# Performance work log

Measured on AMD Instinct MI355X. Metric: run time of the kernel, lower is better.

## Reference

```python
import jax, jax.numpy as jnp
import numpy as np

ND, NM = 20000, 80000
N = ND + NM
IN_D = 256
IN_M = 256
HID = 128
OUT2 = 128  # out_channels * 2
E = 1_600_000
E_TEST = 1_000_000


def setup_inputs() -> dict:
    key = jax.random.key(0)
    ks = jax.random.split(key, 12)
    xd = jax.random.normal(ks[0], (ND, IN_D), jnp.float32)
    xm = jax.random.normal(ks[1], (NM, IN_M), jnp.float32)
    # mlp1: Linear(IN_D, HID); mlp2: Linear(IN_M, HID); gcn: GCNConv(HID, OUT2)
    W1 = jax.random.normal(ks[2], (IN_D, HID), jnp.float32) / np.sqrt(IN_D)
    b1 = jnp.zeros((HID,), jnp.float32)
    W2 = jax.random.normal(ks[3], (IN_M, HID), jnp.float32) / np.sqrt(IN_M)
    b2 = jnp.zeros((HID,), jnp.float32)
    Wg = jax.random.normal(ks[4], (HID, OUT2), jnp.float32) / np.sqrt(HID)
    bg = jnp.zeros((OUT2,), jnp.float32)
    edge_index = jax.random.randint(ks[5], (2, E), 0, N, dtype=jnp.int64)
    edge_index_test = jax.random.randint(ks[6], (2, E_TEST), 0, N, dtype=jnp.int64)
    return dict(xd=xd, xm=xm, edge_index=edge_index, edge_index_test=edge_index_test,
                W1=W1, b1=b1, W2=W2, b2=b2, Wg=Wg, bg=bg)


def gcn_conv(x, edge_index, W, b, num_nodes):
    """PyG GCNConv: x' = D^{-1/2}(A+I)D^{-1/2} x W + b, self-loops added."""
    src, dst = edge_index[0], edge_index[1]
    h = x @ W  # [N, out]
    # degree of A + I (edge weight 1), counted at destination
    deg = jnp.ones((num_nodes,), x.dtype).at[dst].add(1.0)
    norm = jax.lax.rsqrt(deg)
    coef = (norm[src] * norm[dst])[:, None]           # [E,1]
    agg = jax.ops.segment_sum(h[src] * coef, dst, num_segments=num_nodes)
    agg = agg + h * (norm * norm)[:, None]            # self-loop term
    return agg + b


def reference(xd, xm, edge_index, edge_index_test, W1, b1, W2, b2, Wg, bg):
    hd = jax.nn.relu(xd @ W1 + b1)                    # [ND, HID]
    hm = jax.nn.relu(xm @ W2 + b2)                    # [NM, HID]
    x = jnp.concatenate([hd, hm], axis=0)             # [N, HID]
    x = jax.nn.relu(gcn_conv(x, edge_index, Wg, bg, N))  # [N, OUT2]
    # edge dot-product scoring
    scores = jnp.sum(x[edge_index_test[0]] * x[edge_index_test[1]], axis=-1)
    return scores
```

## Files before the change

kernel.cpp:

```cpp
#include <hip/hip_runtime.h>
#include <cstddef>


typedef __attribute__((ext_vector_type(8))) short short8;
typedef __attribute__((ext_vector_type(4))) float f32x4;

#define NBUCK_MAX 2048

__device__ __forceinline__ unsigned short f2bf(float f) {
  union { float f; unsigned u; } v;
  v.f = f;
  unsigned r = v.u + 0x7fffu + ((v.u >> 16) & 1u);
  return (unsigned short)(r >> 16);
}
__device__ __forceinline__ float bf2f(short s) {
  union { unsigned u; float f; } v;
  v.u = ((unsigned)(unsigned short)s) << 16;
  return v.f;
}

__device__ __forceinline__ int eidx(const void* p, int f64, long long i) {
  if (f64) return (int)((const long long*)p)[i];
  return ((const int*)p)[i];
}

__global__ void detect_kernel(const void* __restrict__ ei,
                              const void* __restrict__ eit,
                              int* __restrict__ flags) {
  const unsigned* a = (const unsigned*)ei;
  const unsigned* b = (const unsigned*)eit;
  int f1 = 1, f2 = 1;
  for (int i = 0; i < 64; ++i) {
    if (a[2 * i + 1] != 0u) f1 = 0;
    if (b[2 * i + 1] != 0u) f2 = 0;
  }
  flags[0] = f1;
  flags[1] = f2;
}

__global__ __launch_bounds__(256) void bucket_hist_kernel(
    const void* __restrict__ ei, const int* __restrict__ flags,
    int* __restrict__ bcnt, int E, int nbuck) {
  __shared__ int h[NBUCK_MAX];
  for (int i = threadIdx.x; i < nbuck; i += 256) h[i] = 0;
  __syncthreads();
  int f = flags[0];
  int stride = gridDim.x * 256;
  for (long long e = blockIdx.x * 256 + threadIdx.x; e < E; e += stride) {
    int d = eidx(ei, f, (long long)E + e);
    atomicAdd(&h[d >> 8], 1);
  }
  __syncthreads();
  for (int i = threadIdx.x; i < nbuck; i += 256) {
    int c = h[i];
    if (c) atomicAdd(&bcnt[i], c);
  }
}

__global__ __launch_bounds__(1024) void bucket_scan_kernel(
    const int* __restrict__ bcnt, int* __restrict__ bbase,
    int* __restrict__ bcursor, int nbuck) {
  __shared__ int s[1024];
  int t = threadIdx.x;
  int v = (t < nbuck) ? bcnt[t] : 0;
  s[t] = v;
  __syncthreads();
#pragma unroll
  for (int off = 1; off < 1024; off <<= 1) {
    int x = (t >= off) ? s[t - off] : 0;
    __syncthreads();
    s[t] += x;
    __syncthreads();
  }
  if (t < nbuck) {
    int e = s[t] - v;
    bbase[t] = e;
    bcursor[t] = e;
  }
}

template <int C>
__global__ __launch_bounds__(256) void bin_kernel(
    const void* __restrict__ ei, const int* __restrict__ flags,
    int* __restrict__ bcursor, int* __restrict__ stg, int E, int nbuck) {
  __shared__ int hcnt[NBUCK_MAX];
  __shared__ int hbase[NBUCK_MAX];
  for (int i = threadIdx.x; i < nbuck; i += 256) hcnt[i] = 0;
  __syncthreads();
  int f = flags[0];
  int pk[C], bk[C];
  long long base = (long long)blockIdx.x * 256 * C;
#pragma unroll
  for (int j = 0; j < C; ++j) {
    long long e = base + j * 256 + threadIdx.x;
    if (e < E) {
      int s = eidx(ei, f, e);
      int d = eidx(ei, f, (long long)E + e);
      bk[j] = d >> 8;
      pk[j] = s | ((d & 255) << 20);
      atomicAdd(&hcnt[bk[j]], 1);
    } else {
      bk[j] = -1;
    }
  }
  __syncthreads();
  for (int i = threadIdx.x; i < nbuck; i += 256) {
    int c = hcnt[i];
    hbase[i] = c ? atomicAdd(&bcursor[i], c) : 0;
    hcnt[i] = 0;
  }
  __syncthreads();
#pragma unroll
  for (int j = 0; j < C; ++j) {
    if (bk[j] >= 0) {
      int r = atomicAdd(&hcnt[bk[j]], 1);
      stg[hbase[bk[j]] + r] = pk[j];
    }
  }
}

__global__ __launch_bounds__(256) void sortfin_kernel(
    const int* __restrict__ stg, const int* __restrict__ bbase,
    const int* __restrict__ bcnt, int* __restrict__ sorted_src,
    int* __restrict__ offsets, int* __restrict__ count,
    float* __restrict__ norm, int N) {
  int b = blockIdx.x;
  int start = bbase[b];
  int len = bcnt[b];
  __shared__ int ncnt[256];
  __shared__ int ncur[256];
  __shared__ int stmp[256];
  int t = threadIdx.x;
  ncnt[t] = 0;
  __syncthreads();
  for (int i = t; i < len; i += 256) {
    int p = stg[start + i];
    atomicAdd(&ncnt[p >> 20], 1);
  }
  __syncthreads();
  int c = ncnt[t];
  stmp[t] = c;
  __syncthreads();
#pragma unroll
  for (int off = 1; off < 256; off <<= 1) {
    int x = (t >= off) ? stmp[t - off] : 0;
    __syncthreads();
    stmp[t] += x;
    __syncthreads();
  }
  int aoff = start + stmp[t] - c;
  ncur[t] = aoff;
  int node = (b << 8) + t;
  if (node < N) {
    offsets[node] = aoff;
    count[node] = c;
    norm[node] = rsqrtf((float)c + 1.0f);
  }
  __syncthreads();
  for (int i = t; i < len; i += 256) {
    int p = stg[start + i];
    int pos = atomicAdd(&ncur[p >> 20], 1);
    sorted_src[pos] = p & 0xFFFFF;
  }
}

__global__ void wtrans_all_kernel(const float* __restrict__ W1,
                                  const float* __restrict__ W2,
                                  const float* __restrict__ Wg,
                                  unsigned short* __restrict__ WT1,
                                  unsigned short* __restrict__ WT2,
                                  unsigned short* __restrict__ WTg) {
  int b = blockIdx.x;
  const float* W;
  unsigned short* WT;
  int K, n;
  if (b < 128) {
    W = W1; WT = WT1; K = 256; n = b;
  } else if (b < 256) {
    W = W2; WT = WT2; K = 256; n = b - 128;
  } else {
    W = Wg; WT = WTg; K = 128; n = b - 256;
  }
  for (int k = threadIdx.x; k < K; k += blockDim.x)
    WT[(size_t)n * K + k] = f2bf(W[(size_t)k * 128 + n]);
}

template <int K, bool BF16IN, bool RELU>
__device__ __forceinline__ void gemm_body(const void* __restrict__ Xv,
                                          const unsigned short* __restrict__ WT,
                                          const float* __restrict__ bias,
                                          unsigned short* __restrict__ Yb,
                                          int M, int m0) {
  __shared__ short As[128][40];
  __shared__ short Bs[128][40];

  const int tid = threadIdx.x;
  const int lane = tid & 63;
  const int wave = tid >> 6;
  const int wr = wave >> 1, wc = wave & 1;
  const int lrow = lane & 15;
  const int lk = (lane >> 4) * 8;

  f32x4 acc[4][4];
#pragma unroll
  for (int i = 0; i < 4; ++i)
#pragma unroll
    for (int j = 0; j < 4; ++j) acc[i][j] = (f32x4)(0.0f);

  const int srow = tid >> 1;
  const int skh = (tid & 1) * 16;

  for (int k0 = 0; k0 < K; k0 += 32) {
    {
      int grow = m0 + srow;
      short8 p0 = (short8)(0), p1 = (short8)(0);
      if (grow < M) {
        if (BF16IN) {
          const short* Xb = (const short*)Xv;
          p0 = *(const short8*)&Xb[(size_t)grow * K + k0 + skh];
          p1 = *(const short8*)&Xb[(size_t)grow * K + k0 + skh + 8];
        } else {
          const float* Xf = (const float*)Xv;
          const float4* xp = (const float4*)&Xf[(size_t)grow * K + k0 + skh];
          float4 v0 = xp[0], v1 = xp[1], v2 = xp[2], v3 = xp[3];
          p0[0] = (short)f2bf(v0.x); p0[1] = (short)f2bf(v0.y);
          p0[2] = (short)f2bf(v0.z); p0[3] = (short)f2bf(v0.w);
          p0[4] = (short)f2bf(v1.x); p0[5] = (short)f2bf(v1.y);
          p0[6] = (short)f2bf(v1.z); p0[7] = (short)f2bf(v1.w);
          p1[0] = (short)f2bf(v2.x); p1[1] = (short)f2bf(v2.y);
          p1[2] = (short)f2bf(v2.z); p1[3] = (short)f2bf(v2.w);
          p1[4] = (short)f2bf(v3.x); p1[5] = (short)f2bf(v3.y);
          p1[6] = (short)f2bf(v3.z); p1[7] = (short)f2bf(v3.w);
        }
      }
      *(short8*)&As[srow][skh] = p0;
      *(short8*)&As[srow][skh + 8] = p1;
    }
    {
      const short* wt = (const short*)WT;
      short8 q0 = *(const short8*)&wt[(size_t)srow * K + k0 + skh];
      short8 q1 = *(const short8*)&wt[(size_t)srow * K + k0 + skh + 8];
      *(short8*)&Bs[srow][skh] = q0;
      *(short8*)&Bs[srow][skh + 8] = q1;
    }
    __syncthreads();

    short8 a[4], b[4];
#pragma unroll
    for (int f = 0; f < 4; ++f) {
      a[f] = *(const short8*)&As[wr * 64 + f * 16 + lrow][lk];
      b[f] = *(const short8*)&Bs[wc * 64 + f * 16 + lrow][lk];
    }
#pragma unroll
    for (int fm = 0; fm < 4; ++fm)
#pragma unroll
      for (int fn = 0; fn < 4; ++fn)
        acc[fm][fn] = __builtin_amdgcn_mfma_f32_16x16x32_bf16(
            a[fm], b[fn], acc[fm][fn], 0, 0, 0);
    __syncthreads();
  }

#pragma unroll
  for (int fm = 0; fm < 4; ++fm) {
    int rbase = m0 + wr * 64 + fm * 16 + (lane >> 4) * 4;
#pragma unroll
    for (int fn = 0; fn < 4; ++fn) {
      int col = wc * 64 + fn * 16 + lrow;
      float bv = RELU ? bias[col] : 0.0f;
      f32x4 v = acc[fm][fn];
#pragma unroll
      for (int r = 0; r < 4; ++r) {
        int grow = rbase + r;
        if (grow < M) {
          float x = v[r];
          if (RELU) x = fmaxf(x + bv, 0.0f);
          Yb[(size_t)grow * 128 + col] = f2bf(x);
        }
      }
    }
  }
}

__global__ __launch_bounds__(256) void mlp_gemm_kernel(
    const float* __restrict__ xd, const float* __restrict__ xm,
    const unsigned short* __restrict__ WT1,
    const unsigned short* __restrict__ WT2, const float* __restrict__ b1,
    const float* __restrict__ b2, unsigned short* __restrict__ h, int ND,
    int NM, int nbd) {
  if ((int)blockIdx.x < nbd) {
    gemm_body<256, false, true>(xd, WT1, b1, h, ND, blockIdx.x * 128);
  } else {
    gemm_body<256, false, true>(xm, WT2, b2, h + (size_t)ND * 128, NM,
                                (blockIdx.x - nbd) * 128);
  }
}

__global__ __launch_bounds__(256) void gcn_gemm_kernel(
    const short* __restrict__ h, const unsigned short* __restrict__ WTg,
    unsigned short* __restrict__ h2, int N) {
  gemm_body<128, true, false>(h, WTg, nullptr, h2, N, blockIdx.x * 128);
}

__global__ __launch_bounds__(256) void gather_agg_kernel(
    const short* __restrict__ h2, const float* __restrict__ norm,
    const int* __restrict__ offsets, const int* __restrict__ count,
    const int* __restrict__ sorted_src, const float* __restrict__ bg,
    short* __restrict__ x2, int N) {
  int t = blockIdx.x * blockDim.x + threadIdx.x;
  int node = t >> 3;
  if (node >= N) return;
  int l = t & 7;

  float nd = norm[node];
  int start = offsets[node];
  int len = count[node];

  float a[16];
  {
    short8 s0 = *(const short8*)&h2[(size_t)node * 128 + l * 16];
    short8 s1 = *(const short8*)&h2[(size_t)node * 128 + l * 16 + 8];
    float nw = nd * nd;
#pragma unroll
    for (int i = 0; i < 8; ++i) {
      a[i] = bf2f(s0[i]) * nw;
      a[8 + i] = bf2f(s1[i]) * nw;
    }
  }

  int j = 0;
  for (; j + 2 <= len; j += 2) {
    int sA = sorted_src[start + j];
    int sB = sorted_src[start + j + 1];
    float cA = norm[sA] * nd;
    float cB = norm[sB] * nd;
    const short* pA = &h2[(size_t)sA * 128 + l * 16];
    const short* pB = &h2[(size_t)sB * 128 + l * 16];
    short8 vA0 = *(const short8*)pA;
    short8 vA1 = *(const short8*)(pA + 8);
    short8 vB0 = *(const short8*)pB;
    short8 vB1 = *(const short8*)(pB + 8);
#pragma unroll
    for (int i = 0; i < 8; ++i) {
      a[i] += cA * bf2f(vA0[i]) + cB * bf2f(vB0[i]);
      a[8 + i] += cA * bf2f(vA1[i]) + cB * bf2f(vB1[i]);
    }
  }
  if (j < len) {
    int sA = sorted_src[start + j];
    float cA = norm[sA] * nd;
    const short* pA = &h2[(size_t)sA * 128 + l * 16];
    short8 vA0 = *(const short8*)pA;
    short8 vA1 = *(const short8*)(pA + 8);
#pragma unroll
    for (int i = 0; i < 8; ++i) {
      a[i] += cA * bf2f(vA0[i]);
      a[8 + i] += cA * bf2f(vA1[i]);
    }
  }

  short8 o0, o1;
#pragma unroll
  for (int i = 0; i < 8; ++i) {
    o0[i] = (short)f2bf(fmaxf(a[i] + bg[l * 16 + i], 0.0f));
    o1[i] = (short)f2bf(fmaxf(a[8 + i] + bg[l * 16 + 8 + i], 0.0f));
  }
  *(short8*)&x2[(size_t)node * 128 + l * 16] = o0;
  *(short8*)&x2[(size_t)node * 128 + l * 16 + 8] = o1;
}

__global__ __launch_bounds__(256) void score_kernel(
    const short* __restrict__ x2, const void* __restrict__ eit,
    const int* __restrict__ flags, float* __restrict__ out, int ET) {
  int t = blockIdx.x * blockDim.x + threadIdx.x;
  int e = t >> 3;
  if (e >= ET) return;
  int l = t & 7;
  int f = flags[1];
  int s = eidx(eit, f, e);
  int d = eidx(eit, f, (long long)ET + e);
  const short* pa = &x2[(size_t)s * 128 + l * 16];
  const short* pb = &x2[(size_t)d * 128 + l * 16];
  short8 a0 = *(const short8*)pa;
  short8 a1 = *(const short8*)(pa + 8);
  short8 b0 = *(const short8*)pb;
  short8 b1 = *(const short8*)(pb + 8);
  float p = 0.0f;
#pragma unroll
  for (int i = 0; i < 8; ++i)
    p += bf2f(a0[i]) * bf2f(b0[i]) + bf2f(a1[i]) * bf2f(b1[i]);
  p += __shfl_xor(p, 4);
  p += __shfl_xor(p, 2);
  p += __shfl_xor(p, 1);
  if (l == 0) out[e] = p;
}

extern "C" void kernel_launch(void* const* d_in, const int* in_sizes, int n_in,
                              void* d_out, int out_size, void* d_ws,
                              size_t ws_size, hipStream_t stream) {
  const float* xd = (const float*)d_in[0];
  const float* xm = (const float*)d_in[1];
  const void* ei = d_in[2];
  const void* eit = d_in[3];
  const float* W1 = (const float*)d_in[4];
  const float* b1 = (const float*)d_in[5];
  const float* W2 = (const float*)d_in[6];
  const float* b2 = (const float*)d_in[7];
  const float* Wg = (const float*)d_in[8];
  const float* bg = (const float*)d_in[9];

  const int ND = in_sizes[0] / 256;
  const int NM = in_sizes[1] / 256;
  const int N = ND + NM;
  const int E = in_sizes[2] / 2;
  const int ET = in_sizes[3] / 2;
  const int nbuck = (N + 255) >> 8;

  float* out = (float*)d_out;

  char* p = (char*)d_ws;
  float* norm = (float*)p;        p += (size_t)N * 4;
  int* count = (int*)p;           p += (size_t)N * 4;
  int* offsets = (int*)p;         p += (size_t)N * 4;
  int* bcnt = (int*)p;            p += NBUCK_MAX * 4;
  int* bbase = (int*)p;           p += NBUCK_MAX * 4;
  int* bcursor = (int*)p;         p += NBUCK_MAX * 4;
  int* flags = (int*)p;           p += 16 * 4;
  int* stg = (int*)p;             p += (size_t)E * 4;
  int* sorted_src = (int*)p;      p += (size_t)E * 4;
  p = (char*)(((uintptr_t)p + 15) & ~(uintptr_t)15);
  short* h = (short*)p;           p += (size_t)N * 128 * 2;
  short* h2 = (short*)p;          p += (size_t)N * 128 * 2;
  unsigned short* WT1 = (unsigned short*)p; p += 128 * 256 * 2;
  unsigned short* WT2 = (unsigned short*)p; p += 128 * 256 * 2;
  unsigned short* WTg = (unsigned short*)p; p += 128 * 128 * 2;

  detect_kernel<<<1, 1, 0, stream>>>(ei, eit, flags);
  hipMemsetAsync(bcnt, 0, (size_t)nbuck * 4, stream);

  bucket_hist_kernel<<<256, 256, 0, stream>>>(ei, flags, bcnt, E, nbuck);
  bucket_scan_kernel<<<1, 1024, 0, stream>>>(bcnt, bbase, bcursor, nbuck);
  {
    constexpr int C = 16;
    int nblk = (int)(((long long)E + 256 * C - 1) / (256 * C));
    bin_kernel<C><<<nblk, 256, 0, stream>>>(ei, flags, bcursor, stg, E, nbuck);
  }
  sortfin_kernel<<<nbuck, 256, 0, stream>>>(stg, bbase, bcnt, sorted_src,
                                            offsets, count, norm, N);

  wtrans_all_kernel<<<384, 256, 0, stream>>>(W1, W2, Wg, WT1, WT2, WTg);

  {
    int nbd = (ND + 127) / 128;
    int nbm = (NM + 127) / 128;
    mlp_gemm_kernel<<<nbd + nbm, 256, 0, stream>>>(
        xd, xm, WT1, WT2, b1, b2, (unsigned short*)h, ND, NM, nbd);
  }
  gcn_gemm_kernel<<<(N + 127) / 128, 256, 0, stream>>>(
      h, WTg, (unsigned short*)h2, N);

  {
    long long tt = (long long)N * 8;
    gather_agg_kernel<<<(unsigned)((tt + 255) / 256), 256, 0, stream>>>(
        h2, norm, offsets, count, sorted_src, bg, h, N);
  }

  {
    long long tt = (long long)ET * 8;
    score_kernel<<<(unsigned)((tt + 255) / 256), 256, 0, stream>>>(h, eit, flags,
                                                                   out, ET);
  }
}
```

Before: 298.9 us.

## Co-schedule CSR sort stages with GEMMs via block-range fused kernels

Independent graph-preprocessing stages are merged into the GEMM launches using block-index ranges. Weight transpose and flag detection go in one kernel that also zeroes the bucket counts, replacing the memset. The destination histogram runs alongside the MLP GEMM, and edge binning runs alongside the GCN GEMM. The aggregation loop is also unrolled to four neighbours for more memory parallelism. This cuts launch count and lets memory-bound sorting overlap compute-bound GEMMs, at the cost of larger shared-memory footprints per fused kernel, which may lower occupancy.

```diff
diff --git a/kernel.cpp b/kernel.cpp
--- a/kernel.cpp
+++ b/kernel.cpp
@@ -24,165 +24,40 @@
   return ((const int*)p)[i];
 }
 
-__global__ void detect_kernel(const void* __restrict__ ei,
-                              const void* __restrict__ eit,
-                              int* __restrict__ flags) {
-  const unsigned* a = (const unsigned*)ei;
-  const unsigned* b = (const unsigned*)eit;
-  int f1 = 1, f2 = 1;
-  for (int i = 0; i < 64; ++i) {
-    if (a[2 * i + 1] != 0u) f1 = 0;
-    if (b[2 * i + 1] != 0u) f2 = 0;
-  }
-  flags[0] = f1;
-  flags[1] = f2;
-}
-
-__global__ __launch_bounds__(256) void bucket_hist_kernel(
-    const void* __restrict__ ei, const int* __restrict__ flags,
-    int* __restrict__ bcnt, int E, int nbuck) {
-  __shared__ int h[NBUCK_MAX];
-  for (int i = threadIdx.x; i < nbuck; i += 256) h[i] = 0;
-  __syncthreads();
-  int f = flags[0];
-  int stride = gridDim.x * 256;
-  for (long long e = blockIdx.x * 256 + threadIdx.x; e < E; e += stride) {
-    int d = eidx(ei, f, (long long)E + e);
-    atomicAdd(&h[d >> 8], 1);
-  }
-  __syncthreads();
-  for (int i = threadIdx.x; i < nbuck; i += 256) {
-    int c = h[i];
-    if (c) atomicAdd(&bcnt[i], c);
-  }
-}
-
-__global__ __launch_bounds__(1024) void bucket_scan_kernel(
-    const int* __restrict__ bcnt, int* __restrict__ bbase,
-    int* __restrict__ bcursor, int nbuck) {
-  __shared__ int s[1024];
+__global__ __launch_bounds__(256) void k0_kernel(
+    const float* __restrict__ W1, const float* __restrict__ W2,
+    const float* __restrict__ Wg, unsigned short* __restrict__ WT1,
+    unsigned short* __restrict__ WT2, unsigned short* __restrict__ WTg,
+    const void* __restrict__ ei, const void* __restrict__ eit,
+    int* __restrict__ flags, int* __restrict__ bcnt, int nbuck) {
+  int b = blockIdx.x;
   int t = threadIdx.x;
-  int v = (t < nbuck) ? bcnt[t] : 0;
-  s[t] = v;
-  __syncthreads();
-#pragma unroll
-  for (int off = 1; off < 1024; off <<= 1) {
-    int x = (t >= off) ? s[t - off] : 0;
-    __syncthreads();
-    s[t] += x;
-    __syncthreads();
-  }
-  if (t < nbuck) {
-    int e = s[t] - v;
-    bbase[t] = e;
-    bcursor[t] = e;
-  }
-}
-
-template <int C>
-__global__ __launch_bounds__(256) void bin_kernel(
-    const void* __restrict__ ei, const int* __restrict__ flags,
-    int* __restrict__ bcursor, int* __restrict__ stg, int E, int nbuck) {
-  __shared__ int hcnt[NBUCK_MAX];
-  __shared__ int hbase[NBUCK_MAX];
-  for (int i = threadIdx.x; i < nbuck; i += 256) hcnt[i] = 0;
-  __syncthreads();
-  int f = flags[0];
-  int pk[C], bk[C];
-  long long base = (long long)blockIdx.x * 256 * C;
-#pragma unroll
-  for (int j = 0; j < C; ++j) {
-    long long e = base + j * 256 + threadIdx.x;
-    if (e < E) {
-      int s = eidx(ei, f, e);
-      int d = eidx(ei, f, (long long)E + e);
-      bk[j] = d >> 8;
-      pk[j] = s | ((d & 255) << 20);
-      atomicAdd(&hcnt[bk[j]], 1);
+  if (b < 384) {
+    const float* W;
+    unsigned short* WT;
+    int K, n;
+    if (b < 128) {
+      W = W1; WT = WT1; K = 256; n = b;
+    } else if (b < 256) {
+      W = W2; WT = WT2; K = 256; n = b - 128;
     } else {
-      bk[j] = -1;
-    }
-  }
-  __syncthreads();
-  for (int i = threadIdx.x; i < nbuck; i += 256) {
-    int c = hcnt[i];
-    hbase[i] = c ? atomicAdd(&bcursor[i], c) : 0;
-    hcnt[i] = 0;
-  }
-  __syncthreads();
-#pragma unroll
-  for (int j = 0; j < C; ++j) {
-    if (bk[j] >= 0) {
-      int r = atomicAdd(&hcnt[bk[j]], 1);
-      stg[hbase[bk[j]] + r] = pk[j];
-    }
-  }
-}
-
-__global__ __launch_bounds__(256) void sortfin_kernel(
-    const int* __restrict__ stg, const int* __restrict__ bbase,
-    const int* __restrict__ bcnt, int* __restrict__ sorted_src,
-    int* __restrict__ offsets, int* __restrict__ count,
-    float* __restrict__ norm, int N) {
-  int b = blockIdx.x;
-  int start = bbase[b];
-  int len = bcnt[b];
-  __shared__ int ncnt[256];
-  __shared__ int ncur[256];
-  __shared__ int stmp[256];
-  int t = threadIdx.x;
-  ncnt[t] = 0;
-  __syncthreads();
-  for (int i = t; i < len; i += 256) {
-    int p = stg[start + i];
-    atomicAdd(&ncnt[p >> 20], 1);
-  }
-  __syncthreads();
-  int c = ncnt[t];
-  stmp[t] = c;
-  __syncthreads();
-#pragma unroll
-  for (int off = 1; off < 256; off <<= 1) {
-    int x = (t >= off) ? stmp[t - off] : 0;
-    __syncthreads();
-    stmp[t] += x;
-    __syncthreads();
-  }
-  int aoff = start + stmp[t] - c;
-  ncur[t] = aoff;
-  int node = (b << 8) + t;
-  if (node < N) {
-    offsets[node] = aoff;
-    count[node] = c;
-    norm[node] = rsqrtf((float)c + 1.0f);
-  }
-  __syncthreads();
-  for (int i = t; i < len; i += 256) {
-    int p = stg[start + i];
-    int pos = atomicAdd(&ncur[p >> 20], 1);
-    sorted_src[pos] = p & 0xFFFFF;
-  }
-}
-
-__global__ void wtrans_all_kernel(const float* __restrict__ W1,
-                                  const float* __restrict__ W2,
-                                  const float* __restrict__ Wg,
-                                  unsigned short* __restrict__ WT1,
-                                  unsigned short* __restrict__ WT2,
-                                  unsigned short* __restrict__ WTg) {
-  int b = blockIdx.x;
-  const float* W;
-  unsigned short* WT;
-  int K, n;
-  if (b < 128) {
-    W = W1; WT = WT1; K = 256; n = b;
-  } else if (b < 256) {
-    W = W2; WT = WT2; K = 256; n = b - 128;
+      W = Wg; WT = WTg; K = 128; n = b - 256;
+    }
+    for (int k = t; k < K; k += 256)
+      WT[(size_t)n * K + k] = f2bf(W[(size_t)k * 128 + n]);
   } else {
-    W = Wg; WT = WTg; K = 128; n = b - 256;
-  }
-  for (int k = threadIdx.x; k < K; k += blockDim.x)
-    WT[(size_t)n * K + k] = f2bf(W[(size_t)k * 128 + n]);
+    __shared__ int s1, s2;
+    if (t == 0) { s1 = 1; s2 = 1; }
+    __syncthreads();
+    if (t < 64) {
+      if (((const unsigned*)ei)[2 * t + 1] != 0u) s1 = 0;
+    } else if (t < 128) {
+      if (((const unsigned*)eit)[2 * (t - 64) + 1] != 0u) s2 = 0;
+    }
+    __syncthreads();
+    if (t == 0) { flags[0] = s1; flags[1] = s2; }
+    for (int i = t; i < nbuck; i += 256) bcnt[i] = 0;
+  }
 }
 
 template <int K, bool BF16IN, bool RELU>
@@ -281,24 +156,159 @@
   }
 }
 
-__global__ __launch_bounds__(256) void mlp_gemm_kernel(
+__global__ __launch_bounds__(256) void k1_kernel(
     const float* __restrict__ xd, const float* __restrict__ xm,
     const unsigned short* __restrict__ WT1,
     const unsigned short* __restrict__ WT2, const float* __restrict__ b1,
     const float* __restrict__ b2, unsigned short* __restrict__ h, int ND,
-    int NM, int nbd) {
-  if ((int)blockIdx.x < nbd) {
-    gemm_body<256, false, true>(xd, WT1, b1, h, ND, blockIdx.x * 128);
+    int NM, int nbd, int nbm, const void* __restrict__ ei,
+    const int* __restrict__ flags, int* __restrict__ bcnt, int E, int nbuck) {
+  int b = blockIdx.x;
+  int nmlp = nbd + nbm;
+  if (b < nbd) {
+    gemm_body<256, false, true>(xd, WT1, b1, h, ND, b * 128);
+  } else if (b < nmlp) {
+    gemm_body<256, false, true>(xm, WT2, b2, h + (size_t)ND * 128, NM,
+                                (b - nbd) * 128);
   } else {
-    gemm_body<256, false, true>(xm, WT2, b2, h + (size_t)ND * 128, NM,
-                                (blockIdx.x - nbd) * 128);
-  }
-}
-
-__global__ __launch_bounds__(256) void gcn_gemm_kernel(
+    int rb = b - nmlp;
+    __shared__ int hsh[NBUCK_MAX];
+    for (int i = threadIdx.x; i < nbuck; i += 256) hsh[i] = 0;
+    __syncthreads();
+    int f = flags[0];
+    long long stride = 256LL * 256;
+    for (long long e = (long long)rb * 256 + threadIdx.x; e < E; e += stride) {
+      int d = eidx(ei, f, (long long)E + e);
+      atomicAdd(&hsh[d >> 8], 1);
+    }
+    __syncthreads();
+    for (int i = threadIdx.x; i < nbuck; i += 256) {
+      int c = hsh[i];
+      if (c) atomicAdd(&bcnt[i], c);
+    }
+  }
+}
+
+__global__ __launch_bounds__(1024) void bucket_scan_kernel(
+    const int* __restrict__ bcnt, int* __restrict__ bbase,
+    int* __restrict__ bcursor, int nbuck) {
+  __shared__ int s[1024];
+  int t = threadIdx.x;
+  int v = (t < nbuck) ? bcnt[t] : 0;
+  s[t] = v;
+  __syncthreads();
+#pragma unroll
+  for (int off = 1; off < 1024; off <<= 1) {
+    int x = (t >= off) ? s[t - off] : 0;
+    __syncthreads();
+    s[t] += x;
+    __syncthreads();
+  }
+  if (t < nbuck) {
+    int e = s[t] - v;
+    bbase[t] = e;
+    bcursor[t] = e;
+  }
+}
+
+template <int C>
+__device__ __forceinline__ void bin_body(const void* __restrict__ ei,
+                                         const int* __restrict__ flags,
+                                         int* __restrict__ bcursor,
+                                         int* __restrict__ stg, int E,
+                                         int nbuck, int rb) {
+  __shared__ int hcnt[NBUCK_MAX];
+  __shared__ int hbase[NBUCK_MAX];
+  for (int i = threadIdx.x; i < nbuck; i += 256) hcnt[i] = 0;
+  __syncthreads();
+  int f = flags[0];
+  int pk[C], bk[C];
+  long long base = (long long)rb * 256 * C;
+#pragma unroll
+  for (int j = 0; j < C; ++j) {
+    long long e = base + j * 256 + threadIdx.x;
+    if (e < E) {
+      int s = eidx(ei, f, e);
+      int d = eidx(ei, f, (long long)E + e);
+      bk[j] = d >> 8;
+      pk[j] = s | ((d & 255) << 20);
+      atomicAdd(&hcnt[bk[j]], 1);
+    } else {
+      bk[j] = -1;
+    }
+  }
+  __syncthreads();
+  for (int i = threadIdx.x; i < nbuck; i += 256) {
+    int c = hcnt[i];
+    hbase[i] = c ? atomicAdd(&bcursor[i], c) : 0;
+    hcnt[i] = 0;
+  }
+  __syncthreads();
+#pragma unroll
+  for (int j = 0; j < C; ++j) {
+    if (bk[j] >= 0) {
+      int r = atomicAdd(&hcnt[bk[j]], 1);
+      stg[hbase[bk[j]] + r] = pk[j];
+    }
+  }
+}
+
+__global__ __launch_bounds__(256) void k3_kernel(
     const short* __restrict__ h, const unsigned short* __restrict__ WTg,
-    unsigned short* __restrict__ h2, int N) {
-  gemm_body<128, true, false>(h, WTg, nullptr, h2, N, blockIdx.x * 128);
+    unsigned short* __restrict__ h2, int N, int ngcn,
+    const void* __restrict__ ei, const int* __restrict__ flags,
+    int* __restrict__ bcursor, int* __restrict__ stg, int E, int nbuck) {
+  int b = blockIdx.x;
+  if (b < ngcn) {
+    gemm_body<128, true, false>((const void*)h, WTg, nullptr, h2, N, b * 128);
+  } else {
+    bin_body<16>(ei, flags, bcursor, stg, E, nbuck, b - ngcn);
+  }
+}
+
+__global__ __launch_bounds__(256) void sortfin_kernel(
+    const int* __restrict__ stg, const int* __restrict__ bbase,
+    const int* __restrict__ bcnt, int* __restrict__ sorted_src,
+    int* __restrict__ offsets, int* __restrict__ count,
+    float* __restrict__ norm, int N) {
+  int b = blockIdx.x;
+  int start = bbase[b];
+  int len = bcnt[b];
+  __shared__ int ncnt[256];
+  __shared__ int ncur[256];
+  __shared__ int stmp[256];
+  int t = threadIdx.x;
+  ncnt[t] = 0;
+  __syncthreads();
+  for (int i = t; i < len; i += 256) {
+    int p = stg[start + i];
+    atomicAdd(&ncnt[p >> 20], 1);
+  }
+  __syncthreads();
+  int c = ncnt[t];
+  stmp[t] = c;
+  __syncthreads();
+#pragma unroll
+  for (int off = 1; off < 256; off <<= 1) {
+    int x = (t >= off) ? stmp[t - off] : 0;
+    __syncthreads();
+    stmp[t] += x;
+    __syncthreads();
+  }
+  int aoff = start + stmp[t] - c;
+  ncur[t] = aoff;
+  int node = (b << 8) + t;
+  if (node < N) {
+    offsets[node] = aoff;
+    count[node] = c;
+    norm[node] = rsqrtf((float)c + 1.0f);
+  }
+  __syncthreads();
+  for (int i = t; i < len; i += 256) {
+    int p = stg[start + i];
+    int pos = atomicAdd(&ncur[p >> 20], 1);
+    sorted_src[pos] = p & 0xFFFFF;
+  }
 }
 
 __global__ __launch_bounds__(256) void gather_agg_kernel(
@@ -328,17 +338,37 @@
   }
 
   int j = 0;
+  for (; j + 4 <= len; j += 4) {
+    int sA = sorted_src[start + j];
+    int sB = sorted_src[start + j + 1];
+    int sC = sorted_src[start + j + 2];
+    int sD = sorted_src[start + j + 3];
+    float cA = norm[sA] * nd, cB = norm[sB] * nd;
+    float cC = norm[sC] * nd, cD = norm[sD] * nd;
+    const short* pA = &h2[(size_t)sA * 128 + l * 16];
+    const short* pB = &h2[(size_t)sB * 128 + l * 16];
+    const short* pC = &h2[(size_t)sC * 128 + l * 16];
+    const short* pD = &h2[(size_t)sD * 128 + l * 16];
+    short8 vA0 = *(const short8*)pA, vA1 = *(const short8*)(pA + 8);
+    short8 vB0 = *(const short8*)pB, vB1 = *(const short8*)(pB + 8);
+    short8 vC0 = *(const short8*)pC, vC1 = *(const short8*)(pC + 8);
+    short8 vD0 = *(const short8*)pD, vD1 = *(const short8*)(pD + 8);
+#pragma unroll
+    for (int i = 0; i < 8; ++i) {
+      a[i] += cA * bf2f(vA0[i]) + cB * bf2f(vB0[i]) + cC * bf2f(vC0[i]) +
+              cD * bf2f(vD0[i]);
+      a[8 + i] += cA * bf2f(vA1[i]) + cB * bf2f(vB1[i]) + cC * bf2f(vC1[i]) +
+                  cD * bf2f(vD1[i]);
+    }
+  }
   for (; j + 2 <= len; j += 2) {
     int sA = sorted_src[start + j];
     int sB = sorted_src[start + j + 1];
-    float cA = norm[sA] * nd;
-    float cB = norm[sB] * nd;
+    float cA = norm[sA] * nd, cB = norm[sB] * nd;
     const short* pA = &h2[(size_t)sA * 128 + l * 16];
     const short* pB = &h2[(size_t)sB * 128 + l * 16];
-    short8 vA0 = *(const short8*)pA;
-    short8 vA1 = *(const short8*)(pA + 8);
-    short8 vB0 = *(const short8*)pB;
-    short8 vB1 = *(const short8*)(pB + 8);
+    short8 vA0 = *(const short8*)pA, vA1 = *(const short8*)(pA + 8);
+    short8 vB0 = *(const short8*)pB, vB1 = *(const short8*)(pB + 8);
 #pragma unroll
     for (int i = 0; i < 8; ++i) {
       a[i] += cA * bf2f(vA0[i]) + cB * bf2f(vB0[i]);
@@ -349,8 +379,7 @@
     int sA = sorted_src[start + j];
     float cA = norm[sA] * nd;
     const short* pA = &h2[(size_t)sA * 128 + l * 16];
-    short8 vA0 = *(const short8*)pA;
-    short8 vA1 = *(const short8*)(pA + 8);
+    short8 vA0 = *(const short8*)pA, vA1 = *(const short8*)(pA + 8);
 #pragma unroll
     for (int i = 0; i < 8; ++i) {
       a[i] += cA * bf2f(vA0[i]);
@@ -434,36 +463,27 @@
   unsigned short* WT2 = (unsigned short*)p; p += 128 * 256 * 2;
   unsigned short* WTg = (unsigned short*)p; p += 128 * 128 * 2;
 
-  detect_kernel<<<1, 1, 0, stream>>>(ei, eit, flags);
-  hipMemsetAsync(bcnt, 0, (size_t)nbuck * 4, stream);
-
-  bucket_hist_kernel<<<256, 256, 0, stream>>>(ei, flags, bcnt, E, nbuck);
+  const int nbd = (ND + 127) / 128;
+  const int nbm = (NM + 127) / 128;
+  const int ngcn = (N + 127) / 128;
+  const int nbin = (int)(((long long)E + 4095) / 4096);
+
+  k0_kernel<<<385, 256, 0, stream>>>(W1, W2, Wg, WT1, WT2, WTg, ei, eit, flags,
+                                     bcnt, nbuck);
+  k1_kernel<<<nbd + nbm + 256, 256, 0, stream>>>(
+      xd, xm, WT1, WT2, b1, b2, (unsigned short*)h, ND, NM, nbd, nbm, ei,
+      flags, bcnt, E, nbuck);
   bucket_scan_kernel<<<1, 1024, 0, stream>>>(bcnt, bbase, bcursor, nbuck);
-  {
-    constexpr int C = 16;
-    int nblk = (int)(((long long)E + 256 * C - 1) / (256 * C));
-    bin_kernel<C><<<nblk, 256, 0, stream>>>(ei, flags, bcursor, stg, E, nbuck);
-  }
+  k3_kernel<<<ngcn + nbin, 256, 0, stream>>>(h, WTg, (unsigned short*)h2, N,
+                                             ngcn, ei, flags, bcursor, stg, E,
+                                             nbuck);
   sortfin_kernel<<<nbuck, 256, 0, stream>>>(stg, bbase, bcnt, sorted_src,
                                             offsets, count, norm, N);
-
-  wtrans_all_kernel<<<384, 256, 0, stream>>>(W1, W2, Wg, WT1, WT2, WTg);
-
-  {
-    int nbd = (ND + 127) / 128;
-    int nbm = (NM + 127) / 128;
-    mlp_gemm_kernel<<<nbd + nbm, 256, 0, stream>>>(
-        xd, xm, WT1, WT2, b1, b2, (unsigned short*)h, ND, NM, nbd);
-  }
-  gcn_gemm_kernel<<<(N + 127) / 128, 256, 0, stream>>>(
-      h, WTg, (unsigned short*)h2, N);
-
   {
     long long tt = (long long)N * 8;
     gather_agg_kernel<<<(unsigned)((tt + 255) / 256), 256, 0, stream>>>(
         h2, norm, offsets, count, sorted_src, bg, h, N);
   }
-
   {
     long long tt = (long long)ET * 8;
     score_kernel<<<(unsigned)((tt + 255) / 256), 256, 0, stream>>>(h, eit, flags,
```

After: 274.5 us. -8.2%, faster.
